# Optimization experiments

Hardware: AMD Instinct MI355X
Metric: run time of the kernel (lower is better)

## Reference

```python
import jax, jax.numpy as jnp
import numpy as np

B, N, DM = 8, 1024, 512
H, D = 8, 64  # heads, dim_head; inner_dim = H*D = 512

def setup_inputs() -> dict:
    key = jax.random.key(0)
    k1, k2, k3, k4, k5 = jax.random.split(key, 5)
    s = 1.0 / np.sqrt(DM)
    return {
        "current": jax.random.normal(k1, (B, N, DM), dtype=jnp.float32),
        "hidden": jax.random.normal(k2, (B, N, DM), dtype=jnp.float32),
        "Wq": jax.random.normal(k3, (DM, H * D), dtype=jnp.float32) * s,
        "Wkv": jax.random.normal(k4, (DM, 2 * H * D), dtype=jnp.float32) * s,
        "Wo": jax.random.normal(k5, (H * D, H * D), dtype=jnp.float32) * s,
    }

def reference(current, hidden, Wq, Wkv, Wo):
    b, n, _ = current.shape
    # projections (no bias, matching use_bias=False)
    q = (current @ Wq).reshape(b, n, H, D).transpose(0, 2, 1, 3)   # [B,H,N,D]
    kv = (hidden @ Wkv).reshape(b, n, 2, H, D).transpose(2, 0, 3, 1, 4)  # [2,B,H,N,D]
    k, v = kv[0], kv[1]
    # NOTE: original code computes self.scale but never applies it -> no scaling here
    dots = jnp.einsum('bhqd,bhkd->bhqk', q, k)                      # [B,H,N,N]
    attn = jax.nn.softmax(dots, axis=-1)
    out = jnp.einsum('bhqk,bhkd->bhqd', attn, v)                    # [B,H,N,D]
    out = out.transpose(0, 2, 1, 3).reshape(b, n, H * D)            # [B,N,inner]
    return out @ Wo  # dropout=0.0 -> identity
```

## Files before the change

### kernel.cpp

```cpp
#include <hip/hip_runtime.h>

typedef unsigned short ushort_t;
typedef __attribute__((ext_vector_type(8))) short short8;
typedef __attribute__((ext_vector_type(8))) _Float16 half8;
typedef __attribute__((ext_vector_type(4))) float f32x4;
typedef __attribute__((ext_vector_type(16))) float f32x16;
typedef __attribute__((ext_vector_type(2))) unsigned uint2v;
typedef __attribute__((ext_vector_type(4))) unsigned uint4v;

#define LOG2E 1.44269504088896f

__device__ __forceinline__ void async16(const void* g, void* l) {
  __builtin_amdgcn_global_load_lds(
      (const __attribute__((address_space(1))) void*)g,
      (__attribute__((address_space(3))) void*)l, 16, 0, 0);
}

__device__ __forceinline__ ushort_t f2h(float f) {
  union { _Float16 h; ushort_t u; } c; c.h = (_Float16)f; return c.u;
}

__device__ __forceinline__ half8 u4h8(uint4v u) { union { uint4v a; half8 b; } c; c.a = u; return c.b; }

__device__ __forceinline__ f32x16 zero16() {
  f32x16 v;
  #pragma unroll
  for (int i = 0; i < 16; i++) v[i] = 0.f;
  return v;
}

__global__ __launch_bounds__(256) void prep_all(const float* __restrict__ cur,
                                                const float* __restrict__ hid,
                                                const float* __restrict__ Wq,
                                                const float* __restrict__ Wkv,
                                                const float* __restrict__ Wo,
                                                ushort_t* __restrict__ ch,
                                                ushort_t* __restrict__ hh,
                                                ushort_t* __restrict__ qT,
                                                ushort_t* __restrict__ kvT,
                                                ushort_t* __restrict__ oT) {
  __shared__ float tile[32][33];
  int bid = blockIdx.x;
  if (bid >= 1024) {
    int i = (bid - 1024) * 256 + threadIdx.x;
    const float* src;
    ushort_t* dst;
    int j;
    if (i < 524288) { src = cur; dst = ch; j = i; }
    else            { src = hid; dst = hh; j = i - 524288; }
    const f32x4* s = (const f32x4*)src;
    f32x4 a = s[j * 2], b = s[j * 2 + 1];
    short8 o;
    #pragma unroll
    for (int k = 0; k < 4; k++) {
      o[k] = (short)f2h(a[k]);
      o[k + 4] = (short)f2h(b[k]);
    }
    ((short8*)dst)[j] = o;
    return;
  }
  const float* src; ushort_t* dh; int Nn, bx, by;
  const int K = 512;
  if (bid < 256)      { src = Wq;  dh = qT;  Nn = 512;  bx = (bid & 15) * 32; by = (bid >> 4) * 32; }
  else if (bid < 768) { int b = bid - 256; src = Wkv; dh = kvT; Nn = 1024; bx = (b & 31) * 32; by = (b >> 5) * 32; }
  else                { int b = bid - 768; src = Wo;  dh = oT;  Nn = 512;  bx = (b & 15) * 32; by = (b >> 4) * 32; }
  int tx = threadIdx.x & 31, ty = threadIdx.x >> 5;
  #pragma unroll
  for (int i = 0; i < 32; i += 8)
    tile[ty + i][tx] = src[(size_t)(by + ty + i) * Nn + bx + tx];
  __syncthreads();
  #pragma unroll
  for (int i = 0; i < 32; i += 8) {
    float v = tile[tx][ty + i];
    size_t idx = (size_t)(bx + ty + i) * K + by + tx;
    dh[idx] = f2h(v);
  }
}

template<int EPI, int MT, int TN>
__device__ __forceinline__ void gemm_body(const ushort_t* __restrict__ A,
                                          const ushort_t* __restrict__ B,
                                          ushort_t* __restrict__ o_16,
                                          ushort_t* __restrict__ o_vt,
                                          float* __restrict__ outf,
                                          int K, int ldo, int m0, int n0,
                                          ushort_t* lds) {
  constexpr int BM = MT * 32;
  constexpr int BN = TN * 32;
  constexpr int ASZ = BM * 32;
  constexpr int BSZ = BN * 32;
  constexpr int LPS = (MT + TN) / 2;
  ushort_t* Ash = lds;
  ushort_t* Bsh = lds + 3 * ASZ;
  const int tid = threadIdx.x;
  const int wave = tid >> 6, lane = tid & 63;
  const int wm = (wave >> 1) * (MT * 16), wn = (wave & 1) * (TN * 16);
  const int lrow = lane & 15, lq = lane >> 4;

  f32x4 acc[MT][TN];
  const f32x4 z = {0.f, 0.f, 0.f, 0.f};
  #pragma unroll
  for (int i = 0; i < MT; i++)
    #pragma unroll
    for (int j = 0; j < TN; j++) acc[i][j] = z;

  auto stage = [&](int t, int d) {
    const int k0 = t * 32;
    const int aoff = d * ASZ, boff = d * BSZ;
    #pragma unroll
    for (int i = 0; i < MT / 2; i++) {
      int g = i * 256 + tid;
      int r = g >> 2, kc = g & 3;
      int kcs = kc ^ ((r >> 1) & 3);
      async16(&A[(size_t)(m0 + r) * K + k0 + kcs * 8], &Ash[aoff + g * 8]);
    }
    #pragma unroll
    for (int i = 0; i < TN / 2; i++) {
      int g = i * 256 + tid;
      int r = g >> 2, kc = g & 3;
      int kcs = kc ^ ((r >> 1) & 3);
      async16(&B[(size_t)(n0 + r) * K + k0 + kcs * 8], &Bsh[boff + g * 8]);
    }
  };

  const int nt = K >> 5;
  stage(0, 0);
  stage(1, 1);
  for (int t = 0; t < nt; t++) {
    if (t + 2 < nt) stage(t + 2, (t + 2) % 3);
    if (t + 2 < nt) {
      if constexpr (LPS == 4) asm volatile("s_waitcnt vmcnt(8)" ::: "memory");
      else                    asm volatile("s_waitcnt vmcnt(6)" ::: "memory");
    } else if (t + 1 < nt) {
      if constexpr (LPS == 4) asm volatile("s_waitcnt vmcnt(4)" ::: "memory");
      else                    asm volatile("s_waitcnt vmcnt(3)" ::: "memory");
    } else {
      asm volatile("s_waitcnt vmcnt(0)" ::: "memory");
    }
    __builtin_amdgcn_s_barrier();

    const int d = t % 3;
    const int ab = d * ASZ, bb = d * BSZ;
    half8 af[MT], bf[TN];
    #pragma unroll
    for (int ti = 0; ti < MT; ti++) {
      int row = wm + ti * 16 + lrow;
      af[ti] = *(const half8*)&Ash[ab + row * 32 + (lq ^ ((row >> 1) & 3)) * 8];
    }
    #pragma unroll
    for (int tj = 0; tj < TN; tj++) {
      int row = wn + tj * 16 + lrow;
      bf[tj] = *(const half8*)&Bsh[bb + row * 32 + (lq ^ ((row >> 1) & 3)) * 8];
    }
    #pragma unroll
    for (int ti = 0; ti < MT; ti++)
      #pragma unroll
      for (int tj = 0; tj < TN; tj++)
        acc[ti][tj] = __builtin_amdgcn_mfma_f32_16x16x32_f16(af[ti], bf[tj], acc[ti][tj], 0, 0, 0);

    if (t + 1 < nt) {
      asm volatile("s_waitcnt lgkmcnt(0)" ::: "memory");
      __builtin_amdgcn_s_barrier();
    }
  }

  #pragma unroll
  for (int ti = 0; ti < MT; ti++) {
    #pragma unroll
    for (int tj = 0; tj < TN; tj++) {
      int row0 = m0 + wm + ti * 16 + lq * 4;
      int col = n0 + wn + tj * 16 + lrow;
      #pragma unroll
      for (int r = 0; r < 4; r++) {
        int m = row0 + r;
        float fv = acc[ti][tj][r];
        if (EPI == 0) {
          size_t idx = (size_t)((m >> 10) * 8 + (col >> 6)) * 65536 + (m & 1023) * 64 + (col & 63);
          o_16[idx] = f2h(fv);
        } else if (EPI == 1) {
          if (col < 512) {
            size_t idx = (size_t)((m >> 10) * 8 + (col >> 6)) * 65536 + (m & 1023) * 64 + (col & 63);
            o_16[idx] = f2h(fv);
          } else {
            int cc = col - 512;
            o_vt[(size_t)(((m >> 10) * 8 + (cc >> 6)) * 64 + (cc & 63)) * 1024 + (m & 1023)] = f2h(fv);
          }
        } else {
          outf[(size_t)m * ldo + col] = fv;
        }
      }
    }
  }
}

__global__ __launch_bounds__(256) void gemm_qkv(const ushort_t* __restrict__ H,
                                                const ushort_t* __restrict__ WkvT,
                                                ushort_t* __restrict__ ko,
                                                ushort_t* __restrict__ vt,
                                                const ushort_t* __restrict__ C,
                                                const ushort_t* __restrict__ WqT,
                                                ushort_t* __restrict__ qo) {
  __shared__ __align__(16) ushort_t lds[24576];
  int bid = blockIdx.x;
  int w = (bid & 7) * 96 + (bid >> 3);
  if (w < 512) {
    int n0 = (w & 7) * 128, m0 = (w >> 3) * 128;
    gemm_body<1, 4, 4>(H, WkvT, ko, vt, (float*)nullptr, 512, 0, m0, n0, lds);
  } else {
    int ww = w - 512;
    int n0 = (ww & 3) * 128, m0 = (ww >> 2) * 128;
    gemm_body<0, 4, 4>(C, WqT, qo, (ushort_t*)nullptr, (float*)nullptr, 512, 0, m0, n0, lds);
  }
}

__global__ __launch_bounds__(256) void gemm_o(const ushort_t* __restrict__ A,
                                              const ushort_t* __restrict__ B,
                                              float* __restrict__ outf) {
  __shared__ __align__(16) ushort_t lds[18432];
  int bid = blockIdx.x;
  int w = (bid & 7) * 64 + (bid >> 3);
  int n0 = (w & 3) * 128, m0 = (w >> 2) * 64;
  gemm_body<2, 2, 4>(A, B, (ushort_t*)nullptr, (ushort_t*)nullptr, outf, 512, 512, m0, n0, lds);
}

__global__ __launch_bounds__(256, 2) void flash_attn(const ushort_t* __restrict__ qb,
                                                     const ushort_t* __restrict__ kb,
                                                     const ushort_t* __restrict__ vtb,
                                                     ushort_t* __restrict__ ob) {
  __shared__ __align__(16) ushort_t Ksh[2][64 * 64];
  __shared__ __align__(16) ushort_t VTs[2][64 * 64];

  const int tid = threadIdx.x;
  const int wave = tid >> 6, lane = tid & 63;
  const int bh = blockIdx.x & 63, qt = blockIdx.x >> 6;
  const int l31 = lane & 31, hi = lane >> 5;

  const ushort_t* Q = qb + (size_t)bh * 65536;
  const ushort_t* Kp = kb + (size_t)bh * 65536;
  const ushort_t* VT = vtb + (size_t)bh * 65536;

  const int qrow0 = qt * 128 + wave * 32;

  half8 qf[4];
  #pragma unroll
  for (int ds = 0; ds < 4; ds++)
    qf[ds] = *(const half8*)&Q[(size_t)(qrow0 + l31) * 64 + ds * 16 + hi * 8];

  f32x16 oacc[2];
  oacc[0] = zero16();
  oacc[1] = zero16();
  float m_i = -1e30f, l_i = 0.f;

  const int r7 = l31 & 7;
  int pc[4];
  #pragma unroll
  for (int i = 0; i < 4; i++) pc[i] = (((2 * i + hi) ^ r7) << 3);
  const int ro0 = l31 * 64, ro1 = ro0 + 2048;

  auto stage = [&](int kt, int d) {
    #pragma unroll
    for (int i = 0; i < 2; i++) {
      int g = i * 256 + tid, rw = g >> 3, ch = g & 7;
      int co = ((ch ^ (rw & 7)) << 3);
      int lofs = rw * 64 + (ch << 3);
      async16(&Kp[(size_t)(kt * 64 + rw) * 64 + co], &Ksh[d][lofs]);
      async16(&VT[(size_t)rw * 1024 + kt * 64 + co], &VTs[d][lofs]);
    }
  };

  stage(0, 0);

  for (int kt = 0; kt < 16; kt++) {
    const int cur = kt & 1;
    if (kt < 15) {
      stage(kt + 1, cur ^ 1);
      asm volatile("s_waitcnt vmcnt(4)" ::: "memory");
    } else {
      asm volatile("s_waitcnt vmcnt(0)" ::: "memory");
    }
    __builtin_amdgcn_s_barrier();

    f32x16 sacc0 = zero16(), sacc1 = zero16();
    __builtin_amdgcn_s_setprio(1);
    #pragma unroll
    for (int ds = 0; ds < 4; ds++) {
      half8 k0 = *(const half8*)&Ksh[cur][ro0 + pc[ds]];
      half8 k1 = *(const half8*)&Ksh[cur][ro1 + pc[ds]];
      sacc0 = __builtin_amdgcn_mfma_f32_32x32x16_f16(k0, qf[ds], sacc0, 0, 0, 0);
      sacc1 = __builtin_amdgcn_mfma_f32_32x32x16_f16(k1, qf[ds], sacc1, 0, 0, 0);
    }
    __builtin_amdgcn_s_setprio(0);

    float mx = -1e30f;
    #pragma unroll
    for (int r = 0; r < 16; r++) {
      mx = fmaxf(mx, sacc0[r]);
      mx = fmaxf(mx, sacc1[r]);
    }
    mx = fmaxf(mx, __shfl_xor(mx, 32));
    float mnew = fmaxf(m_i, mx);
    float mL = mnew * LOG2E;
    float alpha = exp2f(fmaf(m_i, LOG2E, -mL));
    float sum = 0.f;
    unsigned pw[16];
    #pragma unroll
    for (int j = 0; j < 8; j++) {
      float p0 = exp2f(fmaf(sacc0[2 * j], LOG2E, -mL));
      float p1 = exp2f(fmaf(sacc0[2 * j + 1], LOG2E, -mL));
      sum += p0 + p1;
      asm("v_cvt_pkrtz_f16_f32 %0, %1, %2" : "=v"(pw[j]) : "v"(p0), "v"(p1));
    }
    #pragma unroll
    for (int j = 0; j < 8; j++) {
      float p0 = exp2f(fmaf(sacc1[2 * j], LOG2E, -mL));
      float p1 = exp2f(fmaf(sacc1[2 * j + 1], LOG2E, -mL));
      sum += p0 + p1;
      asm("v_cvt_pkrtz_f16_f32 %0, %1, %2" : "=v"(pw[8 + j]) : "v"(p0), "v"(p1));
    }
    sum += __shfl_xor(sum, 32);
    l_i = fmaf(l_i, alpha, sum);
    m_i = mnew;
    #pragma unroll
    for (int r = 0; r < 16; r++) {
      oacc[0][r] *= alpha;
      oacc[1][r] *= alpha;
    }

    __builtin_amdgcn_s_setprio(1);
    #pragma unroll
    for (int ks = 0; ks < 4; ks++) {
      const int base = (ks >> 1) * 8 + (ks & 1) * 4;
      uint2v s0 = __builtin_amdgcn_permlane32_swap(pw[base + 0], pw[base + 2], false, false);
      uint2v s1 = __builtin_amdgcn_permlane32_swap(pw[base + 1], pw[base + 3], false, false);
      half8 pfrag = u4h8((uint4v){s0.x, s1.x, s0.y, s1.y});
      half8 vf0 = *(const half8*)&VTs[cur][ro0 + pc[ks]];
      half8 vf1 = *(const half8*)&VTs[cur][ro1 + pc[ks]];
      oacc[0] = __builtin_amdgcn_mfma_f32_32x32x16_f16(vf0, pfrag, oacc[0], 0, 0, 0);
      oacc[1] = __builtin_amdgcn_mfma_f32_32x32x16_f16(vf1, pfrag, oacc[1], 0, 0, 0);
    }
    __builtin_amdgcn_s_setprio(0);

    if (kt < 15) {
      asm volatile("s_waitcnt lgkmcnt(0)" ::: "memory");
      __builtin_amdgcn_s_barrier();
    }
  }

  const int b = bh >> 3, h = bh & 7;
  const int n = qrow0 + l31;
  float rinv = 1.f / l_i;
  #pragma unroll
  for (int dt = 0; dt < 2; dt++) {
    #pragma unroll
    for (int t = 0; t < 4; t++) {
      ushort_t hv[4];
      #pragma unroll
      for (int e = 0; e < 4; e++)
        hv[e] = f2h(oacc[dt][4 * t + e] * rinv);
      size_t idx = (size_t)(b * 1024 + n) * 512 + h * 64 + dt * 32 + t * 8 + hi * 4;
      *(uint2v*)&ob[idx] = (uint2v){(unsigned)hv[0] | ((unsigned)hv[1] << 16),
                                    (unsigned)hv[2] | ((unsigned)hv[3] << 16)};
    }
  }
}

extern "C" void kernel_launch(void* const* d_in, const int* in_sizes, int n_in,
                              void* d_out, int out_size, void* d_ws, size_t ws_size,
                              hipStream_t stream) {
  const float* cur = (const float*)d_in[0];
  const float* hid = (const float*)d_in[1];
  const float* Wq  = (const float*)d_in[2];
  const float* Wkv = (const float*)d_in[3];
  const float* Wo  = (const float*)d_in[4];

  ushort_t* ws = (ushort_t*)d_ws;
  ushort_t* C   = ws;
  ushort_t* H   = C + 4194304;
  ushort_t* ko  = H + 4194304;
  ushort_t* vt  = ko + 4194304;
  ushort_t* qo  = vt + 4194304;
  ushort_t* WqT = qo + 4194304;
  ushort_t* WkvT = WqT + 262144;
  ushort_t* WoT = WkvT + 524288;

  prep_all<<<5120, 256, 0, stream>>>(cur, hid, Wq, Wkv, Wo, C, H, WqT, WkvT, WoT);

  gemm_qkv<<<768, 256, 0, stream>>>(H, WkvT, ko, vt, C, WqT, qo);

  flash_attn<<<512, 256, 0, stream>>>(qo, ko, vt, C);

  gemm_o<<<512, 256, 0, stream>>>(C, WoT, (float*)d_out);
}
```

Measured before the change: 166.5 us.

## Fuse fp32-to-fp16 activation cast into QKV GEMM A-tile loading

The separate pass that converts current/hidden from fp32 to fp16 is removed. The QKV GEMM now loads fp32 A tiles into registers, converts them, and writes them to LDS, with a double-buffered register-staged pipeline in place of the triple-buffered async-to-LDS one. This saves writing and re-reading 16 MB of fp16 activations. In exchange, the GEMM reads fp32 activations (twice the bytes, and each A row is reread by several N tiles), uses more registers, and has a shallower pipeline. The O-projection GEMM is split into its own specialised body.

```diff
diff --git a/kernel.cpp b/kernel.cpp
--- a/kernel.cpp
+++ b/kernel.cpp
@@ -29,36 +29,14 @@
   return v;
 }
 
-__global__ __launch_bounds__(256) void prep_all(const float* __restrict__ cur,
-                                                const float* __restrict__ hid,
-                                                const float* __restrict__ Wq,
-                                                const float* __restrict__ Wkv,
-                                                const float* __restrict__ Wo,
-                                                ushort_t* __restrict__ ch,
-                                                ushort_t* __restrict__ hh,
-                                                ushort_t* __restrict__ qT,
-                                                ushort_t* __restrict__ kvT,
-                                                ushort_t* __restrict__ oT) {
+__global__ __launch_bounds__(256) void prep_w(const float* __restrict__ Wq,
+                                              const float* __restrict__ Wkv,
+                                              const float* __restrict__ Wo,
+                                              ushort_t* __restrict__ qT,
+                                              ushort_t* __restrict__ kvT,
+                                              ushort_t* __restrict__ oT) {
   __shared__ float tile[32][33];
   int bid = blockIdx.x;
-  if (bid >= 1024) {
-    int i = (bid - 1024) * 256 + threadIdx.x;
-    const float* src;
-    ushort_t* dst;
-    int j;
-    if (i < 524288) { src = cur; dst = ch; j = i; }
-    else            { src = hid; dst = hh; j = i - 524288; }
-    const f32x4* s = (const f32x4*)src;
-    f32x4 a = s[j * 2], b = s[j * 2 + 1];
-    short8 o;
-    #pragma unroll
-    for (int k = 0; k < 4; k++) {
-      o[k] = (short)f2h(a[k]);
-      o[k + 4] = (short)f2h(b[k]);
-    }
-    ((short8*)dst)[j] = o;
-    return;
-  }
   const float* src; ushort_t* dh; int Nn, bx, by;
   const int K = 512;
   if (bid < 256)      { src = Wq;  dh = qT;  Nn = 512;  bx = (bid & 15) * 32; by = (bid >> 4) * 32; }
@@ -77,24 +55,21 @@
   }
 }
 
-template<int EPI, int MT, int TN>
-__device__ __forceinline__ void gemm_body(const ushort_t* __restrict__ A,
-                                          const ushort_t* __restrict__ B,
-                                          ushort_t* __restrict__ o_16,
-                                          ushort_t* __restrict__ o_vt,
-                                          float* __restrict__ outf,
-                                          int K, int ldo, int m0, int n0,
-                                          ushort_t* lds) {
-  constexpr int BM = MT * 32;
-  constexpr int BN = TN * 32;
-  constexpr int ASZ = BM * 32;
-  constexpr int BSZ = BN * 32;
-  constexpr int LPS = (MT + TN) / 2;
+template<int EPI>
+__device__ __forceinline__ void gemm_cast_body(const float* __restrict__ A32,
+                                               const ushort_t* __restrict__ B,
+                                               ushort_t* __restrict__ o_16,
+                                               ushort_t* __restrict__ o_vt,
+                                               int K, int m0, int n0,
+                                               ushort_t* lds) {
+  constexpr int MT = 4, TN = 4;
+  constexpr int ASZ = 128 * 32;
+  constexpr int BSZ = 128 * 32;
   ushort_t* Ash = lds;
-  ushort_t* Bsh = lds + 3 * ASZ;
+  ushort_t* Bsh = lds + 2 * ASZ;
   const int tid = threadIdx.x;
   const int wave = tid >> 6, lane = tid & 63;
-  const int wm = (wave >> 1) * (MT * 16), wn = (wave & 1) * (TN * 16);
+  const int wm = (wave >> 1) * 64, wn = (wave & 1) * 64;
   const int lrow = lane & 15, lq = lane >> 4;
 
   f32x4 acc[MT][TN];
@@ -104,43 +79,61 @@
     #pragma unroll
     for (int j = 0; j < TN; j++) acc[i][j] = z;
 
-  auto stage = [&](int t, int d) {
+  f32x4 ar[4];
+
+  auto loadA = [&](int t) {
     const int k0 = t * 32;
-    const int aoff = d * ASZ, boff = d * BSZ;
-    #pragma unroll
-    for (int i = 0; i < MT / 2; i++) {
+    #pragma unroll
+    for (int i = 0; i < 2; i++) {
+      int g = i * 256 + tid, r = g >> 2, kc = g & 3;
+      int kcs = kc ^ ((r >> 1) & 3);
+      const f32x4* p = (const f32x4*)&A32[(size_t)(m0 + r) * K + k0 + kcs * 8];
+      ar[2 * i] = p[0];
+      ar[2 * i + 1] = p[1];
+    }
+  };
+  auto writeA = [&](int d) {
+    #pragma unroll
+    for (int i = 0; i < 2; i++) {
       int g = i * 256 + tid;
-      int r = g >> 2, kc = g & 3;
+      short8 o;
+      #pragma unroll
+      for (int e = 0; e < 4; e++) {
+        o[e] = (short)f2h(ar[2 * i][e]);
+        o[e + 4] = (short)f2h(ar[2 * i + 1][e]);
+      }
+      *(short8*)&Ash[d * ASZ + g * 8] = o;
+    }
+  };
+  auto stageB = [&](int t, int d) {
+    const int k0 = t * 32;
+    #pragma unroll
+    for (int i = 0; i < 2; i++) {
+      int g = i * 256 + tid, r = g >> 2, kc = g & 3;
       int kcs = kc ^ ((r >> 1) & 3);
-      async16(&A[(size_t)(m0 + r) * K + k0 + kcs * 8], &Ash[aoff + g * 8]);
-    }
-    #pragma unroll
-    for (int i = 0; i < TN / 2; i++) {
-      int g = i * 256 + tid;
-      int r = g >> 2, kc = g & 3;
-      int kcs = kc ^ ((r >> 1) & 3);
-      async16(&B[(size_t)(n0 + r) * K + k0 + kcs * 8], &Bsh[boff + g * 8]);
+      async16(&B[(size_t)(n0 + r) * K + k0 + kcs * 8], &Bsh[d * BSZ + g * 8]);
     }
   };
 
+  loadA(0);
+  stageB(0, 0);
+  asm volatile("s_waitcnt vmcnt(2)" ::: "memory");
+  writeA(0);
+  asm volatile("s_waitcnt lgkmcnt(0)" ::: "memory");
+
   const int nt = K >> 5;
-  stage(0, 0);
-  stage(1, 1);
   for (int t = 0; t < nt; t++) {
-    if (t + 2 < nt) stage(t + 2, (t + 2) % 3);
-    if (t + 2 < nt) {
-      if constexpr (LPS == 4) asm volatile("s_waitcnt vmcnt(8)" ::: "memory");
-      else                    asm volatile("s_waitcnt vmcnt(6)" ::: "memory");
-    } else if (t + 1 < nt) {
-      if constexpr (LPS == 4) asm volatile("s_waitcnt vmcnt(4)" ::: "memory");
-      else                    asm volatile("s_waitcnt vmcnt(3)" ::: "memory");
+    const int cur = t & 1;
+    if (t + 1 < nt) {
+      loadA(t + 1);
+      stageB(t + 1, cur ^ 1);
+      asm volatile("s_waitcnt vmcnt(6)" ::: "memory");
     } else {
       asm volatile("s_waitcnt vmcnt(0)" ::: "memory");
     }
     __builtin_amdgcn_s_barrier();
 
-    const int d = t % 3;
-    const int ab = d * ASZ, bb = d * BSZ;
+    const int ab = cur * ASZ, bb = cur * BSZ;
     half8 af[MT], bf[TN];
     #pragma unroll
     for (int ti = 0; ti < MT; ti++) {
@@ -159,6 +152,8 @@
         acc[ti][tj] = __builtin_amdgcn_mfma_f32_16x16x32_f16(af[ti], bf[tj], acc[ti][tj], 0, 0, 0);
 
     if (t + 1 < nt) {
+      asm volatile("s_waitcnt vmcnt(2)" ::: "memory");
+      writeA(cur ^ 1);
       asm volatile("s_waitcnt lgkmcnt(0)" ::: "memory");
       __builtin_amdgcn_s_barrier();
     }
@@ -177,7 +172,7 @@
         if (EPI == 0) {
           size_t idx = (size_t)((m >> 10) * 8 + (col >> 6)) * 65536 + (m & 1023) * 64 + (col & 63);
           o_16[idx] = f2h(fv);
-        } else if (EPI == 1) {
+        } else {
           if (col < 512) {
             size_t idx = (size_t)((m >> 10) * 8 + (col >> 6)) * 65536 + (m & 1023) * 64 + (col & 63);
             o_16[idx] = f2h(fv);
@@ -185,31 +180,115 @@
             int cc = col - 512;
             o_vt[(size_t)(((m >> 10) * 8 + (cc >> 6)) * 64 + (cc & 63)) * 1024 + (m & 1023)] = f2h(fv);
           }
-        } else {
-          outf[(size_t)m * ldo + col] = fv;
         }
       }
     }
   }
 }
 
-__global__ __launch_bounds__(256) void gemm_qkv(const ushort_t* __restrict__ H,
+__global__ __launch_bounds__(256) void gemm_qkv(const float* __restrict__ hid,
                                                 const ushort_t* __restrict__ WkvT,
                                                 ushort_t* __restrict__ ko,
                                                 ushort_t* __restrict__ vt,
-                                                const ushort_t* __restrict__ C,
+                                                const float* __restrict__ cur,
                                                 const ushort_t* __restrict__ WqT,
                                                 ushort_t* __restrict__ qo) {
-  __shared__ __align__(16) ushort_t lds[24576];
+  __shared__ __align__(16) ushort_t lds[16384];
   int bid = blockIdx.x;
   int w = (bid & 7) * 96 + (bid >> 3);
   if (w < 512) {
     int n0 = (w & 7) * 128, m0 = (w >> 3) * 128;
-    gemm_body<1, 4, 4>(H, WkvT, ko, vt, (float*)nullptr, 512, 0, m0, n0, lds);
+    gemm_cast_body<1>(hid, WkvT, ko, vt, 512, m0, n0, lds);
   } else {
     int ww = w - 512;
     int n0 = (ww & 3) * 128, m0 = (ww >> 2) * 128;
-    gemm_body<0, 4, 4>(C, WqT, qo, (ushort_t*)nullptr, (float*)nullptr, 512, 0, m0, n0, lds);
+    gemm_cast_body<0>(cur, WqT, qo, (ushort_t*)nullptr, 512, m0, n0, lds);
+  }
+}
+
+__device__ __forceinline__ void gemm_o_body(const ushort_t* __restrict__ A,
+                                            const ushort_t* __restrict__ B,
+                                            float* __restrict__ outf,
+                                            int K, int ldo, int m0, int n0,
+                                            ushort_t* lds) {
+  constexpr int MT = 2, TN = 4;
+  constexpr int ASZ = 64 * 32;
+  constexpr int BSZ = 128 * 32;
+  ushort_t* Ash = lds;
+  ushort_t* Bsh = lds + 3 * ASZ;
+  const int tid = threadIdx.x;
+  const int wave = tid >> 6, lane = tid & 63;
+  const int wm = (wave >> 1) * 32, wn = (wave & 1) * 64;
+  const int lrow = lane & 15, lq = lane >> 4;
+
+  f32x4 acc[MT][TN];
+  const f32x4 z = {0.f, 0.f, 0.f, 0.f};
+  #pragma unroll
+  for (int i = 0; i < MT; i++)
+    #pragma unroll
+    for (int j = 0; j < TN; j++) acc[i][j] = z;
+
+  auto stage = [&](int t, int d) {
+    const int k0 = t * 32;
+    {
+      int r = tid >> 2, kc = tid & 3;
+      int kcs = kc ^ ((r >> 1) & 3);
+      async16(&A[(size_t)(m0 + r) * K + k0 + kcs * 8], &Ash[d * ASZ + tid * 8]);
+    }
+    #pragma unroll
+    for (int i = 0; i < 2; i++) {
+      int g = i * 256 + tid;
+      int r = g >> 2, kc = g & 3;
+      int kcs = kc ^ ((r >> 1) & 3);
+      async16(&B[(size_t)(n0 + r) * K + k0 + kcs * 8], &Bsh[d * BSZ + g * 8]);
+    }
+  };
+
+  const int nt = K >> 5;
+  stage(0, 0);
+  stage(1, 1);
+  for (int t = 0; t < nt; t++) {
+    if (t + 2 < nt) stage(t + 2, (t + 2) % 3);
+    if (t + 2 < nt)      asm volatile("s_waitcnt vmcnt(6)" ::: "memory");
+    else if (t + 1 < nt) asm volatile("s_waitcnt vmcnt(3)" ::: "memory");
+    else                 asm volatile("s_waitcnt vmcnt(0)" ::: "memory");
+    __builtin_amdgcn_s_barrier();
+
+    const int d = t % 3;
+    const int ab = d * ASZ, bb = d * BSZ;
+    half8 af[MT], bf[TN];
+    #pragma unroll
+    for (int ti = 0; ti < MT; ti++) {
+      int row = wm + ti * 16 + lrow;
+      af[ti] = *(const half8*)&Ash[ab + row * 32 + (lq ^ ((row >> 1) & 3)) * 8];
+    }
+    #pragma unroll
+    for (int tj = 0; tj < TN; tj++) {
+      int row = wn + tj * 16 + lrow;
+      bf[tj] = *(const half8*)&Bsh[bb + row * 32 + (lq ^ ((row >> 1) & 3)) * 8];
+    }
+    #pragma unroll
+    for (int ti = 0; ti < MT; ti++)
+      #pragma unroll
+      for (int tj = 0; tj < TN; tj++)
+        acc[ti][tj] = __builtin_amdgcn_mfma_f32_16x16x32_f16(af[ti], bf[tj], acc[ti][tj], 0, 0, 0);
+
+    if (t + 1 < nt) {
+      asm volatile("s_waitcnt lgkmcnt(0)" ::: "memory");
+      __builtin_amdgcn_s_barrier();
+    }
+  }
+
+  #pragma unroll
+  for (int ti = 0; ti < MT; ti++) {
+    #pragma unroll
+    for (int tj = 0; tj < TN; tj++) {
+      int row0 = m0 + wm + ti * 16 + lq * 4;
+      int col = n0 + wn + tj * 16 + lrow;
+      #pragma unroll
+      for (int r = 0; r < 4; r++)
+        outf[(size_t)(row0 + r) * ldo + col] = acc[ti][tj][r];
+    }
   }
 }
 
@@ -220,7 +299,7 @@
   int bid = blockIdx.x;
   int w = (bid & 7) * 64 + (bid >> 3);
   int n0 = (w & 3) * 128, m0 = (w >> 2) * 64;
-  gemm_body<2, 2, 4>(A, B, (ushort_t*)nullptr, (ushort_t*)nullptr, outf, 512, 512, m0, n0, lds);
+  gemm_o_body(A, B, outf, 512, 512, m0, n0, lds);
 }
 
 __global__ __launch_bounds__(256, 2) void flash_attn(const ushort_t* __restrict__ qb,
@@ -374,20 +453,19 @@
   const float* Wo  = (const float*)d_in[4];
 
   ushort_t* ws = (ushort_t*)d_ws;
-  ushort_t* C   = ws;
-  ushort_t* H   = C + 4194304;
-  ushort_t* ko  = H + 4194304;
+  ushort_t* ko  = ws;
   ushort_t* vt  = ko + 4194304;
   ushort_t* qo  = vt + 4194304;
-  ushort_t* WqT = qo + 4194304;
+  ushort_t* ao  = qo + 4194304;
+  ushort_t* WqT = ao + 4194304;
   ushort_t* WkvT = WqT + 262144;
   ushort_t* WoT = WkvT + 524288;
 
-  prep_all<<<5120, 256, 0, stream>>>(cur, hid, Wq, Wkv, Wo, C, H, WqT, WkvT, WoT);
-
-  gemm_qkv<<<768, 256, 0, stream>>>(H, WkvT, ko, vt, C, WqT, qo);
-
-  flash_attn<<<512, 256, 0, stream>>>(qo, ko, vt, C);
-
-  gemm_o<<<512, 256, 0, stream>>>(C, WoT, (float*)d_out);
-}
+  prep_w<<<1024, 256, 0, stream>>>(Wq, Wkv, Wo, WqT, WkvT, WoT);
+
+  gemm_qkv<<<768, 256, 0, stream>>>(hid, WkvT, ko, vt, cur, WqT, qo);
+
+  flash_attn<<<512, 256, 0, stream>>>(qo, ko, vt, ao);
+
+  gemm_o<<<512, 256, 0, stream>>>(ao, WoT, (float*)d_out);
+}
```

New measurement: 165.9 us. No clear change (-0.4%).

## Enlarge QKV GEMM tiles to 256x256 and skip softmax rescale lazily

Applied to the files above, without the earlier changes.

The QKV projection GEMM now uses 512-thread blocks with 256x256 output tiles, a K-step of 64 with double buffering, and an 8-chunk XOR swizzle, launching 192 blocks instead of 768. The goal is more data reuse per LDS load and fewer global reloads of the operands. The output GEMM keeps its old path through a specialised body. Flash attention now skips rescaling of the running max and accumulator unless some row's max rises by more than a threshold (about 8 in log2 space), which avoids the per-tile multiply of the accumulators. The cost is reliance on fp16 headroom for unnormalised probabilities, and only 192 blocks may leave some of the 256 CUs idle.

```diff
diff --git a/kernel.cpp b/kernel.cpp
--- a/kernel.cpp
+++ b/kernel.cpp
@@ -77,139 +77,196 @@
   }
 }
 
-template<int EPI, int MT, int TN>
-__device__ __forceinline__ void gemm_body(const ushort_t* __restrict__ A,
-                                          const ushort_t* __restrict__ B,
-                                          ushort_t* __restrict__ o_16,
-                                          ushort_t* __restrict__ o_vt,
-                                          float* __restrict__ outf,
-                                          int K, int ldo, int m0, int n0,
-                                          ushort_t* lds) {
-  constexpr int BM = MT * 32;
-  constexpr int BN = TN * 32;
-  constexpr int ASZ = BM * 32;
-  constexpr int BSZ = BN * 32;
-  constexpr int LPS = (MT + TN) / 2;
-  ushort_t* Ash = lds;
-  ushort_t* Bsh = lds + 3 * ASZ;
-  const int tid = threadIdx.x;
-  const int wave = tid >> 6, lane = tid & 63;
-  const int wm = (wave >> 1) * (MT * 16), wn = (wave & 1) * (TN * 16);
-  const int lrow = lane & 15, lq = lane >> 4;
-
-  f32x4 acc[MT][TN];
-  const f32x4 z = {0.f, 0.f, 0.f, 0.f};
-  #pragma unroll
-  for (int i = 0; i < MT; i++)
-    #pragma unroll
-    for (int j = 0; j < TN; j++) acc[i][j] = z;
-
-  auto stage = [&](int t, int d) {
-    const int k0 = t * 32;
-    const int aoff = d * ASZ, boff = d * BSZ;
-    #pragma unroll
-    for (int i = 0; i < MT / 2; i++) {
-      int g = i * 256 + tid;
-      int r = g >> 2, kc = g & 3;
-      int kcs = kc ^ ((r >> 1) & 3);
-      async16(&A[(size_t)(m0 + r) * K + k0 + kcs * 8], &Ash[aoff + g * 8]);
-    }
-    #pragma unroll
-    for (int i = 0; i < TN / 2; i++) {
-      int g = i * 256 + tid;
-      int r = g >> 2, kc = g & 3;
-      int kcs = kc ^ ((r >> 1) & 3);
-      async16(&B[(size_t)(n0 + r) * K + k0 + kcs * 8], &Bsh[boff + g * 8]);
-    }
-  };
-
-  const int nt = K >> 5;
-  stage(0, 0);
-  stage(1, 1);
-  for (int t = 0; t < nt; t++) {
-    if (t + 2 < nt) stage(t + 2, (t + 2) % 3);
-    if (t + 2 < nt) {
-      if constexpr (LPS == 4) asm volatile("s_waitcnt vmcnt(8)" ::: "memory");
-      else                    asm volatile("s_waitcnt vmcnt(6)" ::: "memory");
-    } else if (t + 1 < nt) {
-      if constexpr (LPS == 4) asm volatile("s_waitcnt vmcnt(4)" ::: "memory");
-      else                    asm volatile("s_waitcnt vmcnt(3)" ::: "memory");
-    } else {
-      asm volatile("s_waitcnt vmcnt(0)" ::: "memory");
-    }
-    __builtin_amdgcn_s_barrier();
-
-    const int d = t % 3;
-    const int ab = d * ASZ, bb = d * BSZ;
-    half8 af[MT], bf[TN];
-    #pragma unroll
-    for (int ti = 0; ti < MT; ti++) {
-      int row = wm + ti * 16 + lrow;
-      af[ti] = *(const half8*)&Ash[ab + row * 32 + (lq ^ ((row >> 1) & 3)) * 8];
-    }
-    #pragma unroll
-    for (int tj = 0; tj < TN; tj++) {
-      int row = wn + tj * 16 + lrow;
-      bf[tj] = *(const half8*)&Bsh[bb + row * 32 + (lq ^ ((row >> 1) & 3)) * 8];
-    }
-    #pragma unroll
-    for (int ti = 0; ti < MT; ti++)
-      #pragma unroll
-      for (int tj = 0; tj < TN; tj++)
-        acc[ti][tj] = __builtin_amdgcn_mfma_f32_16x16x32_f16(af[ti], bf[tj], acc[ti][tj], 0, 0, 0);
-
-    if (t + 1 < nt) {
-      asm volatile("s_waitcnt lgkmcnt(0)" ::: "memory");
-      __builtin_amdgcn_s_barrier();
-    }
-  }
-
-  #pragma unroll
-  for (int ti = 0; ti < MT; ti++) {
-    #pragma unroll
-    for (int tj = 0; tj < TN; tj++) {
-      int row0 = m0 + wm + ti * 16 + lq * 4;
-      int col = n0 + wn + tj * 16 + lrow;
-      #pragma unroll
-      for (int r = 0; r < 4; r++) {
-        int m = row0 + r;
-        float fv = acc[ti][tj][r];
-        if (EPI == 0) {
-          size_t idx = (size_t)((m >> 10) * 8 + (col >> 6)) * 65536 + (m & 1023) * 64 + (col & 63);
-          o_16[idx] = f2h(fv);
-        } else if (EPI == 1) {
-          if (col < 512) {
-            size_t idx = (size_t)((m >> 10) * 8 + (col >> 6)) * 65536 + (m & 1023) * 64 + (col & 63);
-            o_16[idx] = f2h(fv);
-          } else {
-            int cc = col - 512;
-            o_vt[(size_t)(((m >> 10) * 8 + (cc >> 6)) * 64 + (cc & 63)) * 1024 + (m & 1023)] = f2h(fv);
-          }
-        } else {
-          outf[(size_t)m * ldo + col] = fv;
-        }
-      }
-    }
-  }
-}
-
-__global__ __launch_bounds__(256) void gemm_qkv(const ushort_t* __restrict__ H,
+__global__ __launch_bounds__(512) void gemm_qkv(const ushort_t* __restrict__ H,
                                                 const ushort_t* __restrict__ WkvT,
                                                 ushort_t* __restrict__ ko,
                                                 ushort_t* __restrict__ vt,
                                                 const ushort_t* __restrict__ C,
                                                 const ushort_t* __restrict__ WqT,
                                                 ushort_t* __restrict__ qo) {
-  __shared__ __align__(16) ushort_t lds[24576];
+  __shared__ __align__(16) ushort_t Ash[2][16384];
+  __shared__ __align__(16) ushort_t Bsh[2][16384];
+  const int tid = threadIdx.x;
+  const int wave = tid >> 6, lane = tid & 63;
+  const int wm = (wave >> 2) * 128, wn = (wave & 3) * 64;
+  const int lrow = lane & 15, lq = lane >> 4;
+  const int K = 512;
+
   int bid = blockIdx.x;
-  int w = (bid & 7) * 96 + (bid >> 3);
-  if (w < 512) {
-    int n0 = (w & 7) * 128, m0 = (w >> 3) * 128;
-    gemm_body<1, 4, 4>(H, WkvT, ko, vt, (float*)nullptr, 512, 0, m0, n0, lds);
-  } else {
-    int ww = w - 512;
-    int n0 = (ww & 3) * 128, m0 = (ww >> 2) * 128;
-    gemm_body<0, 4, 4>(C, WqT, qo, (ushort_t*)nullptr, (float*)nullptr, 512, 0, m0, n0, lds);
+  int w = (bid & 7) * 24 + (bid >> 3);
+  const ushort_t *A, *B;
+  int m0, n0, epi;
+  if (w < 128) { A = H; B = WkvT; m0 = (w >> 2) * 256; n0 = (w & 3) * 256; epi = 1; }
+  else { int ww = w - 128; A = C; B = WqT; m0 = (ww >> 1) * 256; n0 = (ww & 1) * 256; epi = 0; }
+
+  f32x4 acc[8][4];
+  const f32x4 z = {0.f, 0.f, 0.f, 0.f};
+  #pragma unroll
+  for (int i = 0; i < 8; i++)
+    #pragma unroll
+    for (int j = 0; j < 4; j++) acc[i][j] = z;
+
+  auto stage = [&](int t, int d) {
+    const int k0 = t * 64;
+    #pragma unroll
+    for (int i = 0; i < 4; i++) {
+      int g = i * 512 + tid, r = g >> 3, chs = (g & 7) ^ (r & 7);
+      async16(&A[(size_t)(m0 + r) * K + k0 + chs * 8], &Ash[d][g * 8]);
+    }
+    #pragma unroll
+    for (int i = 0; i < 4; i++) {
+      int g = i * 512 + tid, r = g >> 3, chs = (g & 7) ^ (r & 7);
+      async16(&B[(size_t)(n0 + r) * K + k0 + chs * 8], &Bsh[d][g * 8]);
+    }
+  };
+
+  stage(0, 0);
+  for (int t = 0; t < 8; t++) {
+    if (t < 7) {
+      stage(t + 1, (t + 1) & 1);
+      asm volatile("s_waitcnt vmcnt(8)" ::: "memory");
+    } else {
+      asm volatile("s_waitcnt vmcnt(0)" ::: "memory");
+    }
+    __builtin_amdgcn_s_barrier();
+
+    const int d = t & 1;
+    #pragma unroll
+    for (int ks = 0; ks < 2; ks++) {
+      half8 af[8], bf[4];
+      #pragma unroll
+      for (int ti = 0; ti < 8; ti++) {
+        int row = wm + ti * 16 + lrow;
+        af[ti] = *(const half8*)&Ash[d][row * 64 + ((ks * 4 + lq) ^ (row & 7)) * 8];
+      }
+      #pragma unroll
+      for (int tj = 0; tj < 4; tj++) {
+        int row = wn + tj * 16 + lrow;
+        bf[tj] = *(const half8*)&Bsh[d][row * 64 + ((ks * 4 + lq) ^ (row & 7)) * 8];
+      }
+      #pragma unroll
+      for (int ti = 0; ti < 8; ti++)
+        #pragma unroll
+        for (int tj = 0; tj < 4; tj++)
+          acc[ti][tj] = __builtin_amdgcn_mfma_f32_16x16x32_f16(af[ti], bf[tj], acc[ti][tj], 0, 0, 0);
+    }
+
+    if (t < 7) {
+      asm volatile("s_waitcnt lgkmcnt(0)" ::: "memory");
+      __builtin_amdgcn_s_barrier();
+    }
+  }
+
+  #pragma unroll
+  for (int ti = 0; ti < 8; ti++) {
+    #pragma unroll
+    for (int tj = 0; tj < 4; tj++) {
+      int row0 = m0 + wm + ti * 16 + lq * 4;
+      int col = n0 + wn + tj * 16 + lrow;
+      #pragma unroll
+      for (int r = 0; r < 4; r++) {
+        int m = row0 + r;
+        float fv = acc[ti][tj][r];
+        if (epi == 0) {
+          size_t idx = (size_t)((m >> 10) * 8 + (col >> 6)) * 65536 + (m & 1023) * 64 + (col & 63);
+          qo[idx] = f2h(fv);
+        } else {
+          if (col < 512) {
+            size_t idx = (size_t)((m >> 10) * 8 + (col >> 6)) * 65536 + (m & 1023) * 64 + (col & 63);
+            ko[idx] = f2h(fv);
+          } else {
+            int cc = col - 512;
+            vt[(size_t)(((m >> 10) * 8 + (cc >> 6)) * 64 + (cc & 63)) * 1024 + (m & 1023)] = f2h(fv);
+          }
+        }
+      }
+    }
+  }
+}
+
+__device__ __forceinline__ void gemm_o_body(const ushort_t* __restrict__ A,
+                                            const ushort_t* __restrict__ B,
+                                            float* __restrict__ outf,
+                                            int K, int ldo, int m0, int n0,
+                                            ushort_t* lds) {
+  constexpr int MT = 2, TN = 4;
+  constexpr int ASZ = 64 * 32;
+  constexpr int BSZ = 128 * 32;
+  ushort_t* Ash = lds;
+  ushort_t* Bsh = lds + 3 * ASZ;
+  const int tid = threadIdx.x;
+  const int wave = tid >> 6, lane = tid & 63;
+  const int wm = (wave >> 1) * 32, wn = (wave & 1) * 64;
+  const int lrow = lane & 15, lq = lane >> 4;
+
+  f32x4 acc[MT][TN];
+  const f32x4 z = {0.f, 0.f, 0.f, 0.f};
+  #pragma unroll
+  for (int i = 0; i < MT; i++)
+    #pragma unroll
+    for (int j = 0; j < TN; j++) acc[i][j] = z;
+
+  auto stage = [&](int t, int d) {
+    const int k0 = t * 32;
+    {
+      int r = tid >> 2, kc = tid & 3;
+      int kcs = kc ^ ((r >> 1) & 3);
+      async16(&A[(size_t)(m0 + r) * K + k0 + kcs * 8], &Ash[d * ASZ + tid * 8]);
+    }
+    #pragma unroll
+    for (int i = 0; i < 2; i++) {
+      int g = i * 256 + tid;
+      int r = g >> 2, kc = g & 3;
+      int kcs = kc ^ ((r >> 1) & 3);
+      async16(&B[(size_t)(n0 + r) * K + k0 + kcs * 8], &Bsh[d * BSZ + g * 8]);
+    }
+  };
+
+  const int nt = K >> 5;
+  stage(0, 0);
+  stage(1, 1);
+  for (int t = 0; t < nt; t++) {
+    if (t + 2 < nt) stage(t + 2, (t + 2) % 3);
+    if (t + 2 < nt)      asm volatile("s_waitcnt vmcnt(6)" ::: "memory");
+    else if (t + 1 < nt) asm volatile("s_waitcnt vmcnt(3)" ::: "memory");
+    else                 asm volatile("s_waitcnt vmcnt(0)" ::: "memory");
+    __builtin_amdgcn_s_barrier();
+
+    const int d = t % 3;
+    const int ab = d * ASZ, bb = d * BSZ;
+    half8 af[MT], bf[TN];
+    #pragma unroll
+    for (int ti = 0; ti < MT; ti++) {
+      int row = wm + ti * 16 + lrow;
+      af[ti] = *(const half8*)&Ash[ab + row * 32 + (lq ^ ((row >> 1) & 3)) * 8];
+    }
+    #pragma unroll
+    for (int tj = 0; tj < TN; tj++) {
+      int row = wn + tj * 16 + lrow;
+      bf[tj] = *(const half8*)&Bsh[bb + row * 32 + (lq ^ ((row >> 1) & 3)) * 8];
+    }
+    #pragma unroll
+    for (int ti = 0; ti < MT; ti++)
+      #pragma unroll
+      for (int tj = 0; tj < TN; tj++)
+        acc[ti][tj] = __builtin_amdgcn_mfma_f32_16x16x32_f16(af[ti], bf[tj], acc[ti][tj], 0, 0, 0);
+
+    if (t + 1 < nt) {
+      asm volatile("s_waitcnt lgkmcnt(0)" ::: "memory");
+      __builtin_amdgcn_s_barrier();
+    }
+  }
+
+  #pragma unroll
+  for (int ti = 0; ti < MT; ti++) {
+    #pragma unroll
+    for (int tj = 0; tj < TN; tj++) {
+      int row0 = m0 + wm + ti * 16 + lq * 4;
+      int col = n0 + wn + tj * 16 + lrow;
+      #pragma unroll
+      for (int r = 0; r < 4; r++)
+        outf[(size_t)(row0 + r) * ldo + col] = acc[ti][tj][r];
+    }
   }
 }
 
@@ -220,7 +277,7 @@
   int bid = blockIdx.x;
   int w = (bid & 7) * 64 + (bid >> 3);
   int n0 = (w & 3) * 128, m0 = (w >> 2) * 64;
-  gemm_body<2, 2, 4>(A, B, (ushort_t*)nullptr, (ushort_t*)nullptr, outf, 512, 512, m0, n0, lds);
+  gemm_o_body(A, B, outf, 512, 512, m0, n0, lds);
 }
 
 __global__ __launch_bounds__(256, 2) void flash_attn(const ushort_t* __restrict__ qb,
@@ -298,9 +355,20 @@
       mx = fmaxf(mx, sacc1[r]);
     }
     mx = fmaxf(mx, __shfl_xor(mx, 32));
-    float mnew = fmaxf(m_i, mx);
-    float mL = mnew * LOG2E;
-    float alpha = exp2f(fmaf(m_i, LOG2E, -mL));
+
+    if (!__all(mx <= m_i + 5.5451774f)) {
+      float mnew = fmaxf(m_i, mx);
+      float alpha = exp2f((m_i - mnew) * LOG2E);
+      l_i *= alpha;
+      #pragma unroll
+      for (int r = 0; r < 16; r++) {
+        oacc[0][r] *= alpha;
+        oacc[1][r] *= alpha;
+      }
+      m_i = mnew;
+    }
+    float mL = m_i * LOG2E;
+
     float sum = 0.f;
     unsigned pw[16];
     #pragma unroll
@@ -318,13 +386,7 @@
       asm("v_cvt_pkrtz_f16_f32 %0, %1, %2" : "=v"(pw[8 + j]) : "v"(p0), "v"(p1));
     }
     sum += __shfl_xor(sum, 32);
-    l_i = fmaf(l_i, alpha, sum);
-    m_i = mnew;
-    #pragma unroll
-    for (int r = 0; r < 16; r++) {
-      oacc[0][r] *= alpha;
-      oacc[1][r] *= alpha;
-    }
+    l_i += sum;
 
     __builtin_amdgcn_s_setprio(1);
     #pragma unroll
@@ -385,7 +447,7 @@
 
   prep_all<<<5120, 256, 0, stream>>>(cur, hid, Wq, Wkv, Wo, C, H, WqT, WkvT, WoT);
 
-  gemm_qkv<<<768, 256, 0, stream>>>(H, WkvT, ko, vt, C, WqT, qo);
+  gemm_qkv<<<192, 512, 0, stream>>>(H, WkvT, ko, vt, C, WqT, qo);
 
   flash_attn<<<512, 256, 0, stream>>>(qo, ko, vt, C);
 
```

Result: slower. 174.5 us (+4.8%).
